# Performance work log

Measured on AMD Instinct MI355X. Metric: run time of the kernel, lower is better.

Reference implementation:

```python
import jax, jax.numpy as jnp
import numpy as np

ALPHA = 0.2  # LeakyReLU negative slope
NEG_INF = -9.0e15


def setup_inputs() -> dict:
    key = jax.random.key(0)
    k1, k2, k3, k4 = jax.random.split(key, 4)
    B, T, N, Fin, Fout = 2, 8, 2048, 64, 64
    h = jax.random.normal(k1, (B, T, N, Fin), dtype=jnp.float32)
    # xavier_uniform-like init for W [Fin,Fout] and a [2*Fout,1]
    limW = 1.414 * np.sqrt(6.0 / (Fin + Fout))
    W = jax.random.uniform(k2, (Fin, Fout), minval=-limW, maxval=limW, dtype=jnp.float32)
    lima = 1.414 * np.sqrt(6.0 / (2 * Fout + 1))
    a = jax.random.uniform(k3, (2 * Fout, 1), minval=-lima, maxval=lima, dtype=jnp.float32)
    adj = jax.random.randint(k4, (N, N), 0, 2).astype(jnp.int32)
    return {"h": h, "W": W, "a": a, "adj": adj}


def reference(h, W, a, adj):
    Fout = W.shape[1]
    Wh = jnp.matmul(h, W)                      # [B,T,N,Fout]
    Wh1 = jnp.matmul(Wh, a[:Fout])             # [B,T,N,1]
    Wh2 = jnp.matmul(Wh, a[Fout:])             # [B,T,N,1]
    e = Wh1 + jnp.swapaxes(Wh2, -1, -2)        # [B,T,N,N]
    e = jnp.where(e > 0, e, ALPHA * e)         # LeakyReLU
    e = jnp.where(adj > 0, e, jnp.float32(NEG_INF))  # adjacency mask
    # NOTE: source does F.softmax(dim=1) -> softmax over the T axis, replicated faithfully
    attention = jax.nn.softmax(e, axis=1)
    # dropout omitted (eval-mode reference)
    out = jnp.matmul(attention, Wh)            # [B,T,N,Fout]
    return jax.nn.elu(out)                     # concat=True
```

## Files before the change

### kernel.cpp

```cpp
#include <hip/hip_runtime.h>
#include <math.h>

#define B_ 2
#define T_ 8
#define N_ 2048
#define F_ 64
#define TI 32
#define JC 64
#define JCP 72
#define LOG2E 1.44269504088896f
#define PART_STRIDE ((size_t)B_ * T_ * N_ * F_)

typedef __attribute__((ext_vector_type(8))) short short8;
typedef __attribute__((ext_vector_type(4))) float f32x4;

__device__ __forceinline__ unsigned short f2bf(float x) {
  unsigned u = __float_as_uint(x);
  u += 0x7FFFu + ((u >> 16) & 1u);
  return (unsigned short)(u >> 16);
}

__device__ __forceinline__ unsigned cvt_pk_bf16(float lo, float hi) {
  unsigned r;
  asm("v_cvt_pk_bf16_f32 %0, %1, %2" : "=v"(r) : "v"(lo), "v"(hi));
  return r;
}

__device__ __forceinline__ float bf2f(unsigned short u) {
  return __uint_as_float(((unsigned)u) << 16);
}

__global__ __launch_bounds__(256) void prep_kernel(
    const float* __restrict__ h, const float* __restrict__ W,
    const float* __restrict__ a, unsigned short* __restrict__ WhT,
    float* __restrict__ Wh1, float* __restrict__ Wh2) {
  __shared__ float Ws[64][64];
  __shared__ float hs[64][64];
  __shared__ float Whs[64][65];
  const int tid = threadIdx.x;
  const int row0 = blockIdx.x * 64;
  const int bt = row0 >> 11;
  const int j0 = row0 & 2047;
  for (int i = tid; i < 4096; i += 256) Ws[i >> 6][i & 63] = W[i];
  for (int i = tid; i < 4096; i += 256) hs[i >> 6][i & 63] = h[(size_t)row0 * 64 + i];
  __syncthreads();
  const int f = tid & 63;
  const int rq = tid >> 6;
  float acc[16];
#pragma unroll
  for (int m = 0; m < 16; ++m) acc[m] = 0.f;
#pragma unroll 4
  for (int k = 0; k < 64; ++k) {
    const float wvv = Ws[k][f];
#pragma unroll
    for (int m = 0; m < 16; ++m) acc[m] = fmaf(hs[rq * 16 + m][k], wvv, acc[m]);
  }
#pragma unroll
  for (int m = 0; m < 16; ++m) Whs[rq * 16 + m][f] = acc[m];
  __syncthreads();
  {
    const int r = tid >> 2, q = tid & 3;
    float s1 = 0.f, s2 = 0.f;
#pragma unroll
    for (int k = 0; k < 16; ++k) {
      const float v = Whs[r][q * 16 + k];
      s1 = fmaf(v, a[q * 16 + k], s1);
      s2 = fmaf(v, a[64 + q * 16 + k], s2);
    }
    s1 += __shfl_xor(s1, 1); s1 += __shfl_xor(s1, 2);
    s2 += __shfl_xor(s2, 1); s2 += __shfl_xor(s2, 2);
    if (q == 0) {
      Wh1[(size_t)bt * N_ + j0 + r] = s1 * LOG2E;
      Wh2[(size_t)bt * N_ + j0 + r] = s2 * LOG2E;
    }
  }
  {
    const int ff = tid & 63, cp = tid >> 6;
#pragma unroll
    for (int cc = 0; cc < 2; ++cc) {
      const int c = cp * 2 + cc;
      short8 v;
#pragma unroll
      for (int k = 0; k < 8; ++k) v[k] = (short)f2bf(Whs[c * 8 + k][ff]);
      *(short8*)(WhT + ((size_t)bt * 64 + ff) * N_ + j0 + c * 8) = v;
    }
  }
}

__global__ __launch_bounds__(512, 4) void gat_mfma(
    const unsigned short* __restrict__ WhT, const float* __restrict__ Wh1,
    const float* __restrict__ Wh2, const int* __restrict__ adj,
    unsigned short* __restrict__ parts, const int njq) {
  __shared__ unsigned short atts[2][T_][TI][JCP];
  __shared__ float wh2s[2][T_][JC];
  const int tid = threadIdx.x;
  int L = blockIdx.x;
  if (njq == 4) L = (blockIdx.x & 7) * 64 + (blockIdx.x >> 3);
  const int itile = L & 63;
  const int group = L >> 6;
  const int jq = group & (njq - 1);
  const int b = group / njq;
  const int i0 = itile * TI;
  const int jspan = N_ / njq;
  const int jbase = jq * jspan;
  const int nchunk = jspan / JC;

  const int wv = tid >> 6;
  const int lane = tid & 63;
  const int col = lane & 15;
  const int kg = lane >> 4;

  const int sii = tid >> 4;
  const int sjj = (tid & 15) * 4;
  const int st = tid >> 6, sj = tid & 63;

  const unsigned short* wtb = WhT + (size_t)(b * T_ + wv) * F_ * N_;
  const float* wh2b = Wh2 + (size_t)b * T_ * N_;
  const int* adjrow = adj + (size_t)(i0 + sii) * N_ + jbase;

  float w1r[T_];
#pragma unroll
  for (int t = 0; t < T_; ++t) w1r[t] = Wh1[(size_t)(b * T_ + t) * N_ + i0 + sii];

  f32x4 acc[2][4];
#pragma unroll
  for (int it = 0; it < 2; ++it)
#pragma unroll
    for (int nt = 0; nt < 4; ++nt) acc[it][nt] = {0.f, 0.f, 0.f, 0.f};

  wh2s[0][st][sj] = wh2b[(size_t)st * N_ + jbase + sj];
  int4 ad = *(const int4*)(adjrow + sjj);
  __syncthreads();

  for (int c = 0; c < nchunk; ++c) {
    const int j0 = jbase + c * JC;
    const int buf = c & 1;
    short8 breg[4][2];
#pragma unroll
    for (int nt = 0; nt < 4; ++nt)
#pragma unroll
      for (int ks = 0; ks < 2; ++ks)
        breg[nt][ks] = *(const short8*)(wtb + (size_t)(nt * 16 + col) * N_ +
                                        j0 + ks * 32 + kg * 8);
    if (c + 1 < nchunk)
      wh2s[buf ^ 1][st][sj] = wh2b[(size_t)st * N_ + j0 + JC + sj];
    int4 adn = ad;
    if (c + 1 < nchunk) adn = *(const int4*)(adjrow + (c + 1) * JC + sjj);

    {
      float e[T_][4];
      f32x4 s = {0.f, 0.f, 0.f, 0.f};
#pragma unroll
      for (int t = 0; t < T_; ++t) {
        const f32x4 q = *(const f32x4*)(&wh2s[buf][t][sjj]);
#pragma unroll
        for (int cc = 0; cc < 4; ++cc) {
          float x = w1r[t] + q[cc];
          x = fmaxf(x, 0.2f * x);
          e[t][cc] = __builtin_amdgcn_exp2f(x);
          s[cc] += e[t][cc];
        }
      }
      const int adc[4] = {ad.x, ad.y, ad.z, ad.w};
      float rr[4], dd[4];
#pragma unroll
      for (int cc = 0; cc < 4; ++cc) {
        rr[cc] = adc[cc] > 0 ? __builtin_amdgcn_rcpf(s[cc]) : 0.f;
        dd[cc] = adc[cc] > 0 ? 0.f : 0.125f;
      }
#pragma unroll
      for (int t = 0; t < T_; ++t) {
        const float a0 = fmaf(e[t][0], rr[0], dd[0]);
        const float a1 = fmaf(e[t][1], rr[1], dd[1]);
        const float a2 = fmaf(e[t][2], rr[2], dd[2]);
        const float a3 = fmaf(e[t][3], rr[3], dd[3]);
        uint2 w;
        w.x = cvt_pk_bf16(a0, a1);
        w.y = cvt_pk_bf16(a2, a3);
        *(uint2*)&atts[buf][t][sii][sjj] = w;
      }
    }
    ad = adn;
    __syncthreads();
#pragma unroll
    for (int it = 0; it < 2; ++it) {
      const unsigned short* ab = &atts[buf][wv][it * 16 + col][kg * 8];
      const short8 a0 = *(const short8*)ab;
      const short8 a1 = *(const short8*)(ab + 32);
#pragma unroll
      for (int nt = 0; nt < 4; ++nt) {
        acc[it][nt] = __builtin_amdgcn_mfma_f32_16x16x32_bf16(a0, breg[nt][0], acc[it][nt], 0, 0, 0);
        acc[it][nt] = __builtin_amdgcn_mfma_f32_16x16x32_bf16(a1, breg[nt][1], acc[it][nt], 0, 0, 0);
      }
    }
  }

  unsigned short* ob = parts + (size_t)jq * PART_STRIDE +
                       ((size_t)(b * T_ + wv) * N_ + i0) * F_;
#pragma unroll
  for (int it = 0; it < 2; ++it) {
#pragma unroll
    for (int nt = 0; nt < 4; ++nt) {
#pragma unroll
      for (int r = 0; r < 4; ++r) {
        const int row = it * 16 + kg * 4 + r;
        const float x = acc[it][nt][r];
        ob[(size_t)row * F_ + nt * 16 + col] = (unsigned short)cvt_pk_bf16(x, x);
      }
    }
  }
}

__global__ __launch_bounds__(256) void combine_elu(
    float* __restrict__ out, const unsigned short* __restrict__ parts,
    const int njq) {
  const size_t i = ((size_t)blockIdx.x * 256 + threadIdx.x) * 8;
  float s[8] = {0.f, 0.f, 0.f, 0.f, 0.f, 0.f, 0.f, 0.f};
  for (int p = 0; p < njq; ++p) {
    const short8 v = *(const short8*)(parts + (size_t)p * PART_STRIDE + i);
#pragma unroll
    for (int k = 0; k < 8; ++k) s[k] += bf2f((unsigned short)v[k]);
  }
  f32x4 lo, hi;
#pragma unroll
  for (int k = 0; k < 4; ++k) {
    lo[k] = s[k] > 0.f ? s[k] : expm1f(s[k]);
    hi[k] = s[4 + k] > 0.f ? s[4 + k] : expm1f(s[4 + k]);
  }
  *(f32x4*)(out + i) = lo;
  *(f32x4*)(out + i + 4) = hi;
}

extern "C" void kernel_launch(void* const* d_in, const int* in_sizes, int n_in,
                              void* d_out, int out_size, void* d_ws, size_t ws_size,
                              hipStream_t stream) {
  const float* h   = (const float*)d_in[0];
  const float* W   = (const float*)d_in[1];
  const float* a   = (const float*)d_in[2];
  const int*   adj = (const int*)d_in[3];
  float* out = (float*)d_out;

  const size_t whtBytes = (size_t)B_ * T_ * F_ * N_ * 2;
  const size_t vBytes   = (size_t)B_ * T_ * N_ * 4;
  const size_t partB    = PART_STRIDE * 2;

  unsigned short* WhT = (unsigned short*)d_ws;
  float* Wh1 = (float*)((char*)d_ws + whtBytes);
  float* Wh2 = Wh1 + (size_t)B_ * T_ * N_;
  unsigned short* parts = (unsigned short*)(Wh2 + (size_t)B_ * T_ * N_);

  const size_t fixed = whtBytes + 2 * vBytes;
  const int njq = (ws_size >= fixed + 4 * partB) ? 4
                : (ws_size >= fixed + 2 * partB) ? 2 : 1;

  hipLaunchKernelGGL(prep_kernel, dim3(B_ * T_ * N_ / 64), dim3(256), 0, stream,
                     h, W, a, WhT, Wh1, Wh2);
  hipLaunchKernelGGL(gat_mfma, dim3(B_ * (N_ / TI) * njq), dim3(512), 0, stream,
                     WhT, Wh1, Wh2, adj, parts, njq);
  hipLaunchKernelGGL(combine_elu, dim3((unsigned)(PART_STRIDE / (256 * 8))), dim3(256),
                     0, stream, out, parts, njq);
}
```

Baseline: 61.96 us.

## Vectorize prep loads, remap gat block indexing, widen combine per-thread work

The prep kernel now loads W and h into shared memory with 16-byte vector loads instead of scalar loads. The gat_mfma block-to-tile mapping changes so that consecutive blocks cover different j-quarters of the same i-tile, replacing the earlier swizzle. The combine kernel processes 16 elements per thread with half as many blocks, which cuts launch and index overhead but lowers the number of threads in flight. The block remap changes which blocks share adj rows and WhT in cache, so its effect on cache locality could go either way.

```diff
diff --git a/kernel.cpp b/kernel.cpp
--- a/kernel.cpp
+++ b/kernel.cpp
@@ -41,8 +41,10 @@
   const int row0 = blockIdx.x * 64;
   const int bt = row0 >> 11;
   const int j0 = row0 & 2047;
-  for (int i = tid; i < 4096; i += 256) Ws[i >> 6][i & 63] = W[i];
-  for (int i = tid; i < 4096; i += 256) hs[i >> 6][i & 63] = h[(size_t)row0 * 64 + i];
+  for (int i = tid; i < 1024; i += 256)
+    ((f32x4*)Ws)[i] = ((const f32x4*)W)[i];
+  for (int i = tid; i < 1024; i += 256)
+    ((f32x4*)hs)[i] = ((const f32x4*)(h + (size_t)row0 * 64))[i];
   __syncthreads();
   const int f = tid & 63;
   const int rq = tid >> 6;
@@ -94,13 +96,10 @@
   __shared__ unsigned short atts[2][T_][TI][JCP];
   __shared__ float wh2s[2][T_][JC];
   const int tid = threadIdx.x;
-  int L = blockIdx.x;
-  if (njq == 4) L = (blockIdx.x & 7) * 64 + (blockIdx.x >> 3);
-  const int itile = L & 63;
-  const int group = L >> 6;
-  const int jq = group & (njq - 1);
-  const int b = group / njq;
-  const int i0 = itile * TI;
+  const int jq = blockIdx.x % njq;
+  const int rest = blockIdx.x / njq;
+  const int i0 = (rest & 63) * TI;
+  const int b = rest >> 6;
   const int jspan = N_ / njq;
   const int jbase = jq * jspan;
   const int nchunk = jspan / JC;
@@ -214,21 +213,30 @@
 __global__ __launch_bounds__(256) void combine_elu(
     float* __restrict__ out, const unsigned short* __restrict__ parts,
     const int njq) {
-  const size_t i = ((size_t)blockIdx.x * 256 + threadIdx.x) * 8;
-  float s[8] = {0.f, 0.f, 0.f, 0.f, 0.f, 0.f, 0.f, 0.f};
+  const size_t i = ((size_t)blockIdx.x * 256 + threadIdx.x) * 16;
+  float s[16];
+#pragma unroll
+  for (int k = 0; k < 16; ++k) s[k] = 0.f;
   for (int p = 0; p < njq; ++p) {
-    const short8 v = *(const short8*)(parts + (size_t)p * PART_STRIDE + i);
-#pragma unroll
-    for (int k = 0; k < 8; ++k) s[k] += bf2f((unsigned short)v[k]);
-  }
-  f32x4 lo, hi;
-#pragma unroll
-  for (int k = 0; k < 4; ++k) {
-    lo[k] = s[k] > 0.f ? s[k] : expm1f(s[k]);
-    hi[k] = s[4 + k] > 0.f ? s[4 + k] : expm1f(s[4 + k]);
-  }
-  *(f32x4*)(out + i) = lo;
-  *(f32x4*)(out + i + 4) = hi;
+    const unsigned short* pp = parts + (size_t)p * PART_STRIDE + i;
+    const short8 v0 = *(const short8*)(pp);
+    const short8 v1 = *(const short8*)(pp + 8);
+#pragma unroll
+    for (int k = 0; k < 8; ++k) {
+      s[k]     += bf2f((unsigned short)v0[k]);
+      s[8 + k] += bf2f((unsigned short)v1[k]);
+    }
+  }
+#pragma unroll
+  for (int q = 0; q < 4; ++q) {
+    f32x4 r;
+#pragma unroll
+    for (int k = 0; k < 4; ++k) {
+      const float x = s[q * 4 + k];
+      r[k] = x > 0.f ? x : expm1f(x);
+    }
+    *(f32x4*)(out + i + q * 4) = r;
+  }
 }
 
 extern "C" void kernel_launch(void* const* d_in, const int* in_sizes, int n_in,
@@ -257,6 +265,6 @@
                      h, W, a, WhT, Wh1, Wh2);
   hipLaunchKernelGGL(gat_mfma, dim3(B_ * (N_ / TI) * njq), dim3(512), 0, stream,
                      WhT, Wh1, Wh2, adj, parts, njq);
-  hipLaunchKernelGGL(combine_elu, dim3((unsigned)(PART_STRIDE / (256 * 8))), dim3(256),
+  hipLaunchKernelGGL(combine_elu, dim3((unsigned)(PART_STRIDE / (256 * 16))), dim3(256),
                      0, stream, out, parts, njq);
 }
```

Measured after the change: 62.39 us. Within noise of the previous version (+0.7%).
